# Kernel tuning notes

Hardware: AMD Instinct MI355X
Metric: run time of the kernel (lower is better)

The kernel has to match this reference:

```python
import jax, jax.numpy as jnp
import numpy as np

H = 8          # num_heads
DIM = 1024     # embed dim
DH = DIM // H // 2   # per-branch head dim = 64
B, N = 2, 2048
LAMBDA_INIT = 0.5
COS_MIN, COS_MAX = 0.0, 15.0
ALPHA = 0.5            # cos_head_residual_alpha
COS_EPS = 1e-6
RMS_EPS = 1e-5
# raw init so that sigmoid(raw) = (cos_scale_init - min)/(max - min) = 1/15
RAW_INIT = float(np.log((1.0/15.0) / (1.0 - 1.0/15.0)))


def setup_inputs() -> dict:
    key = jax.random.key(0)
    ks = jax.random.split(key, 10)
    s = 1.0 / np.sqrt(DIM)
    return {
        "x": jax.random.normal(ks[0], (B, N, DIM), jnp.float32),
        "Wq": jax.random.normal(ks[1], (DIM, DIM), jnp.float32) * s,
        "Wk": jax.random.normal(ks[2], (DIM, DIM), jnp.float32) * s,
        "Wv": jax.random.normal(ks[3], (DIM, DIM), jnp.float32) * s,
        "Wo": jax.random.normal(ks[4], (DIM, DIM), jnp.float32) * s,
        "bo": jnp.zeros((DIM,), jnp.float32),
        "lambda_q1": jax.random.normal(ks[5], (DH,), jnp.float32) * 0.1,
        "lambda_k1": jax.random.normal(ks[6], (DH,), jnp.float32) * 0.1,
        "lambda_q2": jax.random.normal(ks[7], (DH,), jnp.float32) * 0.1,
        "lambda_k2": jax.random.normal(ks[8], (DH,), jnp.float32) * 0.1,
        "delta_gain": jax.random.normal(ks[9], (H,), jnp.float32) * 0.1,
        "cos_head_delta": jnp.zeros((H,), jnp.float32),
        "cos_logit_scale_raw": jnp.float32(RAW_INIT),
        "subln_weight": jnp.ones((2 * DH,), jnp.float32),
    }


def _l2norm(t):
    # F.normalize: x / max(||x||_2, eps)
    return t / jnp.maximum(jnp.linalg.norm(t, axis=-1, keepdims=True), COS_EPS)


def reference(x, Wq, Wk, Wv, Wo, bo,
              lambda_q1, lambda_k1, lambda_q2, lambda_k2,
              delta_gain, cos_head_delta, cos_logit_scale_raw, subln_weight):
    b, n, c = x.shape
    # projections (torch Linear: x @ W.T)
    q = (x @ Wq.T).reshape(b, n, H, 2, DH).transpose(0, 2, 3, 1, 4)  # (B,H,2,N,Dh)
    k = (x @ Wk.T).reshape(b, n, H, 2, DH).transpose(0, 2, 3, 1, 4)
    v = (x @ Wv.T).reshape(b, n, H, 2 * DH).transpose(0, 2, 1, 3)    # (B,H,N,2Dh)
    q1, q2 = q[:, :, 0], q[:, :, 1]
    k1, k2 = k[:, :, 0], k[:, :, 1]

    # smooth-bounded cosine logit scale with per-head residual
    gscale = COS_MIN + (COS_MAX - COS_MIN) * jax.nn.sigmoid(cos_logit_scale_raw)
    head_delta = cos_head_delta - cos_head_delta.mean()
    cos_scale = (gscale * (1.0 + ALPHA * jnp.tanh(head_delta))).reshape(1, H, 1, 1)

    L1 = jnp.einsum('bhnd,bhmd->bhnm', _l2norm(q1), _l2norm(k1)) * cos_scale
    L2 = jnp.einsum('bhnd,bhmd->bhnm', _l2norm(q2), _l2norm(k2)) * cos_scale
    L1 = jnp.nan_to_num(L1)
    L2 = jnp.nan_to_num(L2)

    # tanh-gated interaction between branches
    G = jnp.tanh(delta_gain.reshape(1, H, 1, 1) * (L1 - L2))
    A1 = jax.nn.softmax((L1 + G).astype(jnp.float32), axis=-1).astype(x.dtype)
    A2 = jax.nn.softmax((L2 - G).astype(jnp.float32), axis=-1).astype(x.dtype)

    lambda_1 = jnp.exp(jnp.sum(lambda_q1 * lambda_k1))
    lambda_2 = jnp.exp(jnp.sum(lambda_q2 * lambda_k2))
    lambda_full = (lambda_1 - lambda_2 + LAMBDA_INIT).astype(x.dtype)

    attn = A1 - lambda_full * A2
    y = jnp.einsum('bhnm,bhmd->bhnd', attn, v)  # (B,H,N,2Dh)

    # sub-layer RMSNorm over last dim (2*Dh) with affine weight
    y = y * jax.lax.rsqrt(jnp.mean(y * y, axis=-1, keepdims=True) + RMS_EPS) * subln_weight
    y = y * (1.0 - LAMBDA_INIT)

    y = y.transpose(0, 2, 1, 3).reshape(b, n, c)
    return y @ Wo.T + bo
```

## Files before the change

kernel.cpp:

```cpp
#include <hip/hip_runtime.h>
#include <hip/hip_bf16.h>
#include <cstdint>

typedef __attribute__((ext_vector_type(8))) short short8_t;
typedef __attribute__((ext_vector_type(4))) float f32x4;
typedef __attribute__((ext_vector_type(16))) float f32x16;

#define LOG2E 1.4426950408889634f

__device__ __forceinline__ ushort f2bf(float f){
  union { float f; uint32_t i; } x; x.f = f;
  uint32_t r = x.i + 0x7FFFu + ((x.i >> 16) & 1u);
  return (ushort)(r >> 16);
}
__device__ __forceinline__ float fexp2(float x){
  float r; asm("v_exp_f32 %0, %1" : "=v"(r) : "v"(x)); return r;
}
__device__ __forceinline__ uint32_t cvtpk_bf16(float lo, float hi){
  uint32_t r;
  asm("v_cvt_pk_bf16_f32 %0, %1, %2" : "=v"(r) : "v"(lo), "v"(hi));
  return r;
}
__device__ __forceinline__ void pl32swap(uint32_t &a, uint32_t &b){
  asm volatile("v_permlane32_swap_b32 %0, %1" : "+v"(a), "+v"(b));
}
union PF { uint32_t u[4]; short8_t v; };

__global__ __launch_bounds__(256) void cvt_all_kernel(const float* __restrict__ x,
                                                      const float* __restrict__ Wq,
                                                      const float* __restrict__ Wk,
                                                      const float* __restrict__ Wv,
                                                      const float* __restrict__ Wo,
                                                      ushort* __restrict__ xb,
                                                      ushort* __restrict__ wqb,
                                                      ushort* __restrict__ wkb,
                                                      ushort* __restrict__ wvb,
                                                      ushort* __restrict__ wob){
  int bid = blockIdx.x;
  const float* s; ushort* d; int i;
  if (bid < 4096){ s = x; d = xb; i = bid * 256 + threadIdx.x; }
  else {
    int sel = (bid - 4096) >> 10;
    s = sel == 0 ? Wq : sel == 1 ? Wk : sel == 2 ? Wv : Wo;
    d = sel == 0 ? wqb : sel == 1 ? wkb : sel == 2 ? wvb : wob;
    i = ((bid - 4096) & 1023) * 256 + threadIdx.x;
  }
  float4 v = ((const float4*)s)[i];
  ushort4 o;
  o.x = f2bf(v.x); o.y = f2bf(v.y); o.z = f2bf(v.z); o.w = f2bf(v.w);
  ((ushort4*)d)[i] = o;
}

__global__ void prep_kernel(const float* __restrict__ lq1, const float* __restrict__ lk1,
                            const float* __restrict__ lq2, const float* __restrict__ lk2,
                            const float* __restrict__ dgain, const float* __restrict__ chd,
                            const float* __restrict__ rawp, float* __restrict__ sc){
  int lane = threadIdx.x;
  float p1 = lq1[lane] * lk1[lane];
  float p2 = lq2[lane] * lk2[lane];
  #pragma unroll
  for (int o = 1; o < 64; o <<= 1){
    p1 += __shfl_xor(p1, o, 64);
    p2 += __shfl_xor(p2, o, 64);
  }
  if (lane == 0) sc[24] = expf(p1) - expf(p2) + 0.5f;
  if (lane < 8){
    float m = 0.f;
    for (int i = 0; i < 8; i++) m += chd[i];
    m *= 0.125f;
    float gs = 15.f / (1.f + expf(-rawp[0]));
    float cs = gs * (1.f + 0.5f * tanhf(chd[lane] - m));
    sc[lane]      = LOG2E * cs;
    sc[8 + lane]  = LOG2E * (cs + 1.f);
    sc[16 + lane] = 2.f * dgain[lane];
  }
}

__global__ __launch_bounds__(256) void gemm_qkv(const ushort* __restrict__ A,
                                                const ushort* __restrict__ wqb,
                                                const ushort* __restrict__ wkb,
                                                const ushort* __restrict__ wvb,
                                                ushort* __restrict__ Qs,
                                                ushort* __restrict__ Kn,
                                                ushort* __restrict__ Vt,
                                                const float* __restrict__ sc){
  constexpr int N = 1024, K = 1024;
  __shared__ ushort As[128*32];
  __shared__ ushort Bs[128*32];
  const int z = blockIdx.z;
  const ushort* Bm = z == 0 ? wqb : (z == 1 ? wkb : wvb);
  const int t = threadIdx.x;
  const int lane = t & 63;
  const int w = t >> 6;
  const int wr = w >> 1, wc = w & 1;
  const long Ar0 = (long)blockIdx.x * 128;
  const long Br0 = (long)blockIdx.y * 128;
  const int r15 = lane & 15;
  const int kb = (lane >> 4) * 8;

  f32x4 acc[4][4];
  #pragma unroll
  for (int m = 0; m < 4; m++)
    #pragma unroll
    for (int n = 0; n < 4; n++) acc[m][n] = (f32x4){0.f, 0.f, 0.f, 0.f};

  for (int k0 = 0; k0 < K; k0 += 32){
    __syncthreads();
    #pragma unroll
    for (int r = 0; r < 2; r++){
      int li = r * 256 + t;
      int row = li >> 2;
      int col = (li & 3) * 8;
      __builtin_amdgcn_global_load_lds(
        (const __attribute__((address_space(1))) uint32_t*)(A + (Ar0 + row) * K + k0 + col),
        (__attribute__((address_space(3))) uint32_t*)(As + li * 8), 16, 0, 0);
      __builtin_amdgcn_global_load_lds(
        (const __attribute__((address_space(1))) uint32_t*)(Bm + (Br0 + row) * K + k0 + col),
        (__attribute__((address_space(3))) uint32_t*)(Bs + li * 8), 16, 0, 0);
    }
    __syncthreads();
    short8_t af[4], bfv[4];
    #pragma unroll
    for (int m = 0; m < 4; m++) af[m]  = *(const short8_t*)(As + (wr*64 + m*16 + r15)*32 + kb);
    #pragma unroll
    for (int n = 0; n < 4; n++) bfv[n] = *(const short8_t*)(Bs + (wc*64 + n*16 + r15)*32 + kb);
    #pragma unroll
    for (int m = 0; m < 4; m++)
      #pragma unroll
      for (int n = 0; n < 4; n++)
        acc[m][n] = __builtin_amdgcn_mfma_f32_16x16x32_bf16(af[m], bfv[n], acc[m][n], 0, 0, 0);
  }

  const int fr = (lane >> 4) * 4;
  if (z == 2){
    #pragma unroll
    for (int m = 0; m < 4; m++){
      #pragma unroll
      for (int n = 0; n < 4; n++){
        long row0 = Ar0 + wr*64 + m*16 + fr;
        long col  = Br0 + wc*64 + n*16 + r15;
        int bidx = (int)(row0 >> 11);
        int tok  = (int)(row0 & 2047);
        int hh   = (int)(col >> 7);
        int dd   = (int)(col & 127);
        ushort4 pk;
        pk.x = f2bf(acc[m][n][0]); pk.y = f2bf(acc[m][n][1]);
        pk.z = f2bf(acc[m][n][2]); pk.w = f2bf(acc[m][n][3]);
        *(ushort4*)(Vt + ((long)((bidx*8 + hh)*128 + dd))*2048 + tok) = pk;
      }
    }
  } else {
    ushort* dst = (z == 0) ? Qs : Kn;
    const float qsc = (z == 0) ? sc[Br0 >> 7] : 1.f;
    #pragma unroll
    for (int m = 0; m < 4; m++){
      float ss[4] = {0.f, 0.f, 0.f, 0.f};
      #pragma unroll
      for (int n = 0; n < 4; n++)
        #pragma unroll
        for (int r = 0; r < 4; r++) ss[r] = fmaf(acc[m][n][r], acc[m][n][r], ss[r]);
      #pragma unroll
      for (int r = 0; r < 4; r++){
        ss[r] += __shfl_xor(ss[r], 1, 16);
        ss[r] += __shfl_xor(ss[r], 2, 16);
        ss[r] += __shfl_xor(ss[r], 4, 16);
        ss[r] += __shfl_xor(ss[r], 8, 16);
        ss[r] = qsc / fmaxf(sqrtf(ss[r]), 1e-6f);
      }
      long row0 = Ar0 + wr*64 + m*16 + fr;
      #pragma unroll
      for (int n = 0; n < 4; n++){
        long col = Br0 + wc*64 + n*16 + r15;
        #pragma unroll
        for (int r = 0; r < 4; r++)
          dst[(row0 + r) * N + col] = f2bf(acc[m][n][r] * ss[r]);
      }
    }
  }
}

__global__ __launch_bounds__(256) void gemm_o(const ushort* __restrict__ A,
                                              const ushort* __restrict__ Bm,
                                              float* __restrict__ Cout,
                                              const float* __restrict__ bias){
  constexpr int N = 1024, K = 1024;
  __shared__ ushort As[128*32];
  __shared__ ushort Bs[128*32];
  const int t = threadIdx.x;
  const int lane = t & 63;
  const int w = t >> 6;
  const int wr = w >> 1, wc = w & 1;
  const long Ar0 = (long)blockIdx.x * 128;
  const long Br0 = (long)blockIdx.y * 128;
  const int r15 = lane & 15;
  const int kb = (lane >> 4) * 8;

  f32x4 acc[4][4];
  #pragma unroll
  for (int m = 0; m < 4; m++)
    #pragma unroll
    for (int n = 0; n < 4; n++) acc[m][n] = (f32x4){0.f, 0.f, 0.f, 0.f};

  for (int k0 = 0; k0 < K; k0 += 32){
    __syncthreads();
    #pragma unroll
    for (int r = 0; r < 2; r++){
      int li = r * 256 + t;
      int row = li >> 2;
      int col = (li & 3) * 8;
      __builtin_amdgcn_global_load_lds(
        (const __attribute__((address_space(1))) uint32_t*)(A + (Ar0 + row) * K + k0 + col),
        (__attribute__((address_space(3))) uint32_t*)(As + li * 8), 16, 0, 0);
      __builtin_amdgcn_global_load_lds(
        (const __attribute__((address_space(1))) uint32_t*)(Bm + (Br0 + row) * K + k0 + col),
        (__attribute__((address_space(3))) uint32_t*)(Bs + li * 8), 16, 0, 0);
    }
    __syncthreads();
    short8_t af[4], bfv[4];
    #pragma unroll
    for (int m = 0; m < 4; m++) af[m]  = *(const short8_t*)(As + (wr*64 + m*16 + r15)*32 + kb);
    #pragma unroll
    for (int n = 0; n < 4; n++) bfv[n] = *(const short8_t*)(Bs + (wc*64 + n*16 + r15)*32 + kb);
    #pragma unroll
    for (int m = 0; m < 4; m++)
      #pragma unroll
      for (int n = 0; n < 4; n++)
        acc[m][n] = __builtin_amdgcn_mfma_f32_16x16x32_bf16(af[m], bfv[n], acc[m][n], 0, 0, 0);
  }

  const int fr = (lane >> 4) * 4;
  #pragma unroll
  for (int m = 0; m < 4; m++){
    #pragma unroll
    for (int n = 0; n < 4; n++){
      long row0 = Ar0 + wr*64 + m*16 + fr;
      long col  = Br0 + wc*64 + n*16 + r15;
      float bsv = bias[col];
      #pragma unroll
      for (int r = 0; r < 4; r++)
        Cout[(row0 + r) * N + col] = acc[m][n][r] + bsv;
    }
  }
}

__device__ __forceinline__ void stage256(const ushort* __restrict__ Kn,
                                         const ushort* __restrict__ Vt,
                                         long kslice, long vslice, int ktAbs,
                                         ushort* buf, int t){
  #pragma unroll
  for (int r = 0; r < 4; r++){
    int s = r * 256 + t;
    int key = s >> 4, ci = s & 15;
    const ushort* srcK = Kn + kslice + (long)(ktAbs + key) * 1024 + ((ci ^ (key & 15)) * 8);
    __builtin_amdgcn_global_load_lds(
      (const __attribute__((address_space(1))) uint32_t*)srcK,
      (__attribute__((address_space(3))) uint32_t*)(buf + s * 8), 16, 0, 0);
    int dim = s >> 3, ci2 = s & 7;
    const ushort* srcV = Vt + vslice + (long)dim * 2048 + ktAbs + ((ci2 ^ (dim & 7)) * 8);
    __builtin_amdgcn_global_load_lds(
      (const __attribute__((address_space(1))) uint32_t*)srcV,
      (__attribute__((address_space(3))) uint32_t*)(buf + 64*128 + s * 8), 16, 0, 0);
  }
}

__global__ __launch_bounds__(256, 2) void attn5_kernel(
    const ushort* __restrict__ Qs, const ushort* __restrict__ Kn,
    const ushort* __restrict__ Vt, ushort* __restrict__ Yb,
    const float* __restrict__ sc, const float* __restrict__ subw){
  __shared__ ushort KV[2][64*128 + 128*64];
  __shared__ float Zb[2][2][64];
  const int t = threadIdx.x;
  const int w = t >> 6;
  const int l = t & 63;
  const int lo5 = l & 31;
  const int hi = l >> 5;
  const int qt = w >> 1;
  const int kp = w & 1;
  const int bh = blockIdx.y;
  const int b = bh >> 3, h = bh & 7;
  const int q0 = blockIdx.x * 64 + qt * 32;
  const float dgh2 = sc[16 + h];
  const float shl  = sc[8 + h];
  const float lam  = sc[24];

  short8_t qf[8];
  {
    const ushort* qp = Qs + (long)(b*2048 + q0 + lo5) * 1024 + h*128 + hi*8;
    #pragma unroll
    for (int c = 0; c < 2; c++)
      #pragma unroll
      for (int kc = 0; kc < 4; kc++)
        qf[c*4 + kc] = *(const short8_t*)(qp + c*64 + kc*16);
  }

  f32x16 y1a[4], y2a[4];
  #pragma unroll
  for (int nt = 0; nt < 4; nt++)
    #pragma unroll
    for (int i = 0; i < 16; i++){ y1a[nt][i] = 0.f; y2a[nt][i] = 0.f; }
  float Z1 = 0.f, Z2 = 0.f;

  const long kslice = (long)b * 2048 * 1024 + h * 128;
  const long vslice = (long)(b*8 + h) * 128 * 2048;

  for (int kt0 = 0; kt0 < 1024; kt0 += 64){
    __syncthreads();
    stage256(Kn, Vt, kslice, vslice, kt0,        KV[0], t);
    stage256(Kn, Vt, kslice, vslice, 1024 + kt0, KV[1], t);
    __syncthreads();
    const ushort* Ks = KV[kp];
    const ushort* Vs = KV[kp] + 64*128;

    #pragma unroll
    for (int step = 0; step < 2; step++){
      const int key = step*32 + lo5;
      const int krow = key * 128;
      const int ksw = key & 15;
      f32x16 s1, s2;
      #pragma unroll
      for (int i = 0; i < 16; i++){ s1[i] = 0.f; s2[i] = 0.f; }
      #pragma unroll
      for (int kc = 0; kc < 4; kc++){
        short8_t kf = *(const short8_t*)(Ks + krow + (((kc*2 + hi) ^ ksw) * 8));
        s1 = __builtin_amdgcn_mfma_f32_32x32x16_bf16(kf, qf[kc], s1, 0, 0, 0);
      }
      #pragma unroll
      for (int kc = 0; kc < 4; kc++){
        short8_t kf = *(const short8_t*)(Ks + krow + (((8 + kc*2 + hi) ^ ksw) * 8));
        s2 = __builtin_amdgcn_mfma_f32_32x32x16_bf16(kf, qf[4 + kc], s2, 0, 0, 0);
      }

      uint32_t pa1[8], pa2[8];
      #pragma unroll
      for (int ks = 0; ks < 2; ks++){
        #pragma unroll
        for (int u = 0; u < 2; u++){
          const int rr = 8*ks + 2*u;
          float e1[4], e2[4];
          #pragma unroll
          for (int g4 = 0; g4 < 4; g4++){
            const int r = rr + (g4 >> 1)*4 + (g4 & 1);
            float a = s1[r], c = s2[r];
            float e  = fexp2(dgh2 * (a - c));
            float rc = __builtin_amdgcn_rcpf(e + 1.f);
            float gl = fmaf(-2.f * LOG2E, rc, LOG2E);
            float p1 = fexp2(a + gl - shl);
            float p2 = fexp2(c - gl - shl);
            Z1 += p1; Z2 += p2;
            e1[g4] = p1; e2[g4] = p2;
          }
          uint32_t a1 = cvtpk_bf16(e1[0], e1[1]), b1 = cvtpk_bf16(e1[2], e1[3]);
          uint32_t a2 = cvtpk_bf16(e2[0], e2[1]), b2 = cvtpk_bf16(e2[2], e2[3]);
          pl32swap(a1, b1);
          pl32swap(a2, b2);
          pa1[ks*4 + u] = a1; pa1[ks*4 + 2 + u] = b1;
          pa2[ks*4 + u] = a2; pa2[ks*4 + 2 + u] = b2;
        }
      }

      #pragma unroll
      for (int ks = 0; ks < 2; ks++){
        PF f1, f2;
        #pragma unroll
        for (int i = 0; i < 4; i++){ f1.u[i] = pa1[ks*4 + i]; f2.u[i] = pa2[ks*4 + i]; }
        const int ck = step*4 + ks*2 + hi;
        #pragma unroll
        for (int nt = 0; nt < 4; nt++){
          const int dim = nt*32 + lo5;
          short8_t vf = *(const short8_t*)(Vs + dim*64 + ((ck ^ (dim & 7)) * 8));
          y1a[nt] = __builtin_amdgcn_mfma_f32_32x32x16_bf16(f1.v, vf, y1a[nt], 0, 0, 0);
          y2a[nt] = __builtin_amdgcn_mfma_f32_32x32x16_bf16(f2.v, vf, y2a[nt], 0, 0, 0);
        }
      }
    }
  }

  Z1 += __shfl_xor(Z1, 32, 64);
  Z2 += __shfl_xor(Z2, 32, 64);

  __syncthreads();
  float* Mb = (float*)(&KV[0][0]);
  if (kp == 1){
    #pragma unroll
    for (int nt = 0; nt < 4; nt++)
      #pragma unroll
      for (int i = 0; i < 16; i++){
        Mb[(((qt*2 + 0)*4 + nt)*16 + i)*64 + l] = y1a[nt][i];
        Mb[(((qt*2 + 1)*4 + nt)*16 + i)*64 + l] = y2a[nt][i];
      }
    Zb[qt][0][l] = Z1; Zb[qt][1][l] = Z2;
  }
  __syncthreads();
  if (kp == 1) return;

  #pragma unroll
  for (int nt = 0; nt < 4; nt++)
    #pragma unroll
    for (int i = 0; i < 16; i++){
      y1a[nt][i] += Mb[(((qt*2 + 0)*4 + nt)*16 + i)*64 + l];
      y2a[nt][i] += Mb[(((qt*2 + 1)*4 + nt)*16 + i)*64 + l];
    }
  Z1 += Zb[qt][0][l];
  Z2 += Zb[qt][1][l];

  #pragma unroll
  for (int r = 0; r < 16; r++){
    const int qr = (r & 3) + 8*(r >> 2) + 4*hi;
    float z1r = __shfl(Z1, (l & 32) | qr, 64);
    float z2r = __shfl(Z2, (l & 32) | qr, 64);
    float inv1 = 1.f / z1r;
    float inv2 = lam / z2r;
    float yv[4]; float ssq = 0.f;
    #pragma unroll
    for (int nt = 0; nt < 4; nt++){
      yv[nt] = y1a[nt][r]*inv1 - y2a[nt][r]*inv2;
      ssq = fmaf(yv[nt], yv[nt], ssq);
    }
    ssq += __shfl_xor(ssq, 1, 64);
    ssq += __shfl_xor(ssq, 2, 64);
    ssq += __shfl_xor(ssq, 4, 64);
    ssq += __shfl_xor(ssq, 8, 64);
    ssq += __shfl_xor(ssq, 16, 64);
    float rms = rsqrtf(ssq * (1.f / 128.f) + 1e-5f);
    const long tok = (long)b*2048 + q0 + qr;
    ushort* op = Yb + tok*1024 + h*128;
    #pragma unroll
    for (int nt = 0; nt < 4; nt++){
      const int dim = nt*32 + lo5;
      op[dim] = f2bf(yv[nt] * rms * subw[dim] * 0.5f);
    }
  }
}

extern "C" void kernel_launch(void* const* d_in, const int* in_sizes, int n_in,
                              void* d_out, int out_size, void* d_ws, size_t ws_size,
                              hipStream_t stream) {
  const float* x   = (const float*)d_in[0];
  const float* Wq  = (const float*)d_in[1];
  const float* Wk  = (const float*)d_in[2];
  const float* Wv  = (const float*)d_in[3];
  const float* Wo  = (const float*)d_in[4];
  const float* bo  = (const float*)d_in[5];
  const float* lq1 = (const float*)d_in[6];
  const float* lk1 = (const float*)d_in[7];
  const float* lq2 = (const float*)d_in[8];
  const float* lk2 = (const float*)d_in[9];
  const float* dg  = (const float*)d_in[10];
  const float* chd = (const float*)d_in[11];
  const float* raw = (const float*)d_in[12];
  const float* subw= (const float*)d_in[13];
  float* out = (float*)d_out;

  char* ws = (char*)d_ws;
  const size_t MB = 1024 * 1024;
  ushort* xb  = (ushort*)(ws);
  ushort* wqb = (ushort*)(ws + 8 * MB);
  ushort* wkb = wqb + 1024 * 1024;
  ushort* wvb = wkb + 1024 * 1024;
  ushort* wob = wvb + 1024 * 1024;
  ushort* Qs  = (ushort*)(ws + 16 * MB);
  ushort* Kn  = Qs + 4 * 1024 * 1024;
  ushort* Vt  = Kn + 4 * 1024 * 1024;
  ushort* Yb  = Vt + 4 * 1024 * 1024;
  float*  sc  = (float*)(Yb + 4 * 1024 * 1024);

  cvt_all_kernel<<<8192, 256, 0, stream>>>(x, Wq, Wk, Wv, Wo, xb, wqb, wkb, wvb, wob);
  prep_kernel<<<1, 64, 0, stream>>>(lq1, lk1, lq2, lk2, dg, chd, raw, sc);

  gemm_qkv<<<dim3(32, 8, 3), 256, 0, stream>>>(xb, wqb, wkb, wvb, Qs, Kn, Vt, sc);

  attn5_kernel<<<dim3(32, 16), 256, 0, stream>>>(Qs, Kn, Vt, Yb, sc, subw);

  gemm_o<<<dim3(32, 8), 256, 0, stream>>>(Yb, wob, out, bo);
}
```

Baseline: 164.1 us.

## Double-buffer K/V tiles in attention to overlap prefetch with compute

The attention kernel now stages 32-key K/V tiles into two alternating LDS buffers. It issues the async global-to-LDS loads for the next tile right after a single barrier, then computes on the current tile, replacing the old load-then-barrier-then-compute pattern that had two barriers per 64-key step. The V swizzle is reworked for the narrower 32-key tile, and load offsets are precomputed once outside the loop. It also drops the per-head constant log-shift subtraction before exp2. That saves one op per element, but it relies on the bounded cosine logits to avoid overflow.

```diff
diff --git a/kernel.cpp b/kernel.cpp
--- a/kernel.cpp
+++ b/kernel.cpp
@@ -243,31 +243,11 @@
   }
 }
 
-__device__ __forceinline__ void stage256(const ushort* __restrict__ Kn,
-                                         const ushort* __restrict__ Vt,
-                                         long kslice, long vslice, int ktAbs,
-                                         ushort* buf, int t){
-  #pragma unroll
-  for (int r = 0; r < 4; r++){
-    int s = r * 256 + t;
-    int key = s >> 4, ci = s & 15;
-    const ushort* srcK = Kn + kslice + (long)(ktAbs + key) * 1024 + ((ci ^ (key & 15)) * 8);
-    __builtin_amdgcn_global_load_lds(
-      (const __attribute__((address_space(1))) uint32_t*)srcK,
-      (__attribute__((address_space(3))) uint32_t*)(buf + s * 8), 16, 0, 0);
-    int dim = s >> 3, ci2 = s & 7;
-    const ushort* srcV = Vt + vslice + (long)dim * 2048 + ktAbs + ((ci2 ^ (dim & 7)) * 8);
-    __builtin_amdgcn_global_load_lds(
-      (const __attribute__((address_space(1))) uint32_t*)srcV,
-      (__attribute__((address_space(3))) uint32_t*)(buf + 64*128 + s * 8), 16, 0, 0);
-  }
-}
-
-__global__ __launch_bounds__(256, 2) void attn5_kernel(
+__global__ __launch_bounds__(256, 2) void attn6_kernel(
     const ushort* __restrict__ Qs, const ushort* __restrict__ Kn,
     const ushort* __restrict__ Vt, ushort* __restrict__ Yb,
     const float* __restrict__ sc, const float* __restrict__ subw){
-  __shared__ ushort KV[2][64*128 + 128*64];
+  __shared__ ushort KV[2][2][8192];
   __shared__ float Zb[2][2][64];
   const int t = threadIdx.x;
   const int w = t >> 6;
@@ -280,8 +260,8 @@
   const int b = bh >> 3, h = bh & 7;
   const int q0 = blockIdx.x * 64 + qt * 32;
   const float dgh2 = sc[16 + h];
-  const float shl  = sc[8 + h];
   const float lam  = sc[24];
+  const int f2 = (lo5 & 3) ^ ((lo5 >> 2) & 3);
 
   short8_t qf[8];
   {
@@ -303,74 +283,103 @@
   const long kslice = (long)b * 2048 * 1024 + h * 128;
   const long vslice = (long)(b*8 + h) * 128 * 2048;
 
-  for (int kt0 = 0; kt0 < 1024; kt0 += 64){
+  int koff[2], kdst[2], voff[2], vdst[2];
+  #pragma unroll
+  for (int r = 0; r < 2; r++){
+    int c = r * 256 + t;
+    int key = c >> 4, ci = c & 15;
+    kdst[r] = c * 8;
+    koff[r] = key * 1024 + ((ci ^ (key & 15)) * 8);
+    int dim = c >> 2, ci2 = c & 3;
+    int fv = (dim & 3) ^ ((dim >> 2) & 3);
+    vdst[r] = 4096 + c * 8;
+    voff[r] = dim * 2048 + ((ci2 ^ fv) * 8);
+  }
+
+  auto stage = [&](int tileKp, int buf, int ktAbs){
+    const ushort* bk = Kn + kslice + (long)ktAbs * 1024;
+    const ushort* bv = Vt + vslice + ktAbs;
+    ushort* dst = &KV[tileKp][buf][0];
+    #pragma unroll
+    for (int r = 0; r < 2; r++){
+      __builtin_amdgcn_global_load_lds(
+        (const __attribute__((address_space(1))) uint32_t*)(bk + koff[r]),
+        (__attribute__((address_space(3))) uint32_t*)(dst + kdst[r]), 16, 0, 0);
+      __builtin_amdgcn_global_load_lds(
+        (const __attribute__((address_space(1))) uint32_t*)(bv + voff[r]),
+        (__attribute__((address_space(3))) uint32_t*)(dst + vdst[r]), 16, 0, 0);
+    }
+  };
+
+  stage(0, 0, 0);
+  stage(1, 0, 1024);
+  int buf = 0;
+  for (int it = 0; it < 32; it++, buf ^= 1){
     __syncthreads();
-    stage256(Kn, Vt, kslice, vslice, kt0,        KV[0], t);
-    stage256(Kn, Vt, kslice, vslice, 1024 + kt0, KV[1], t);
-    __syncthreads();
-    const ushort* Ks = KV[kp];
-    const ushort* Vs = KV[kp] + 64*128;
-
-    #pragma unroll
-    for (int step = 0; step < 2; step++){
-      const int key = step*32 + lo5;
-      const int krow = key * 128;
-      const int ksw = key & 15;
-      f32x16 s1, s2;
-      #pragma unroll
-      for (int i = 0; i < 16; i++){ s1[i] = 0.f; s2[i] = 0.f; }
-      #pragma unroll
-      for (int kc = 0; kc < 4; kc++){
-        short8_t kf = *(const short8_t*)(Ks + krow + (((kc*2 + hi) ^ ksw) * 8));
-        s1 = __builtin_amdgcn_mfma_f32_32x32x16_bf16(kf, qf[kc], s1, 0, 0, 0);
-      }
-      #pragma unroll
-      for (int kc = 0; kc < 4; kc++){
-        short8_t kf = *(const short8_t*)(Ks + krow + (((8 + kc*2 + hi) ^ ksw) * 8));
-        s2 = __builtin_amdgcn_mfma_f32_32x32x16_bf16(kf, qf[4 + kc], s2, 0, 0, 0);
-      }
-
-      uint32_t pa1[8], pa2[8];
-      #pragma unroll
-      for (int ks = 0; ks < 2; ks++){
+    if (it + 1 < 32){
+      stage(0, buf ^ 1, (it + 1) * 32);
+      stage(1, buf ^ 1, 1024 + (it + 1) * 32);
+    }
+    const ushort* Ks = &KV[kp][buf][0];
+    const ushort* Vs = &KV[kp][buf][4096];
+
+    const int key = lo5;
+    const int krow = key * 128;
+    const int ksw = key & 15;
+    f32x16 s1, s2;
+    #pragma unroll
+    for (int i = 0; i < 16; i++){ s1[i] = 0.f; s2[i] = 0.f; }
+    #pragma unroll
+    for (int kc = 0; kc < 4; kc++){
+      short8_t kf = *(const short8_t*)(Ks + krow + (((kc*2 + hi) ^ ksw) * 8));
+      s1 = __builtin_amdgcn_mfma_f32_32x32x16_bf16(kf, qf[kc], s1, 0, 0, 0);
+    }
+    #pragma unroll
+    for (int kc = 0; kc < 4; kc++){
+      short8_t kf = *(const short8_t*)(Ks + krow + (((8 + kc*2 + hi) ^ ksw) * 8));
+      s2 = __builtin_amdgcn_mfma_f32_32x32x16_bf16(kf, qf[4 + kc], s2, 0, 0, 0);
+    }
+
+    uint32_t pa1[8], pa2[8];
+    #pragma unroll
+    for (int ks = 0; ks < 2; ks++){
+      #pragma unroll
+      for (int u = 0; u < 2; u++){
+        const int rr = 8*ks + 2*u;
+        float e1[4], e2[4];
         #pragma unroll
-        for (int u = 0; u < 2; u++){
-          const int rr = 8*ks + 2*u;
-          float e1[4], e2[4];
-          #pragma unroll
-          for (int g4 = 0; g4 < 4; g4++){
-            const int r = rr + (g4 >> 1)*4 + (g4 & 1);
-            float a = s1[r], c = s2[r];
-            float e  = fexp2(dgh2 * (a - c));
-            float rc = __builtin_amdgcn_rcpf(e + 1.f);
-            float gl = fmaf(-2.f * LOG2E, rc, LOG2E);
-            float p1 = fexp2(a + gl - shl);
-            float p2 = fexp2(c - gl - shl);
-            Z1 += p1; Z2 += p2;
-            e1[g4] = p1; e2[g4] = p2;
-          }
-          uint32_t a1 = cvtpk_bf16(e1[0], e1[1]), b1 = cvtpk_bf16(e1[2], e1[3]);
-          uint32_t a2 = cvtpk_bf16(e2[0], e2[1]), b2 = cvtpk_bf16(e2[2], e2[3]);
-          pl32swap(a1, b1);
-          pl32swap(a2, b2);
-          pa1[ks*4 + u] = a1; pa1[ks*4 + 2 + u] = b1;
-          pa2[ks*4 + u] = a2; pa2[ks*4 + 2 + u] = b2;
+        for (int g4 = 0; g4 < 4; g4++){
+          const int r = rr + (g4 >> 1)*4 + (g4 & 1);
+          float a = s1[r], c = s2[r];
+          float e  = fexp2(dgh2 * (a - c));
+          float rc = __builtin_amdgcn_rcpf(e + 1.f);
+          float gl = fmaf(-2.f * LOG2E, rc, LOG2E);
+          float p1 = fexp2(a + gl);
+          float p2 = fexp2(c - gl);
+          Z1 += p1; Z2 += p2;
+          e1[g4] = p1; e2[g4] = p2;
         }
-      }
-
-      #pragma unroll
-      for (int ks = 0; ks < 2; ks++){
-        PF f1, f2;
-        #pragma unroll
-        for (int i = 0; i < 4; i++){ f1.u[i] = pa1[ks*4 + i]; f2.u[i] = pa2[ks*4 + i]; }
-        const int ck = step*4 + ks*2 + hi;
-        #pragma unroll
-        for (int nt = 0; nt < 4; nt++){
-          const int dim = nt*32 + lo5;
-          short8_t vf = *(const short8_t*)(Vs + dim*64 + ((ck ^ (dim & 7)) * 8));
-          y1a[nt] = __builtin_amdgcn_mfma_f32_32x32x16_bf16(f1.v, vf, y1a[nt], 0, 0, 0);
-          y2a[nt] = __builtin_amdgcn_mfma_f32_32x32x16_bf16(f2.v, vf, y2a[nt], 0, 0, 0);
-        }
+        uint32_t a1 = cvtpk_bf16(e1[0], e1[1]), b1 = cvtpk_bf16(e1[2], e1[3]);
+        uint32_t a2 = cvtpk_bf16(e2[0], e2[1]), b2 = cvtpk_bf16(e2[2], e2[3]);
+        pl32swap(a1, b1);
+        pl32swap(a2, b2);
+        pa1[ks*4 + u] = a1; pa1[ks*4 + 2 + u] = b1;
+        pa2[ks*4 + u] = a2; pa2[ks*4 + 2 + u] = b2;
+      }
+    }
+
+    #pragma unroll
+    for (int ks = 0; ks < 2; ks++){
+      PF pf1, pf2;
+      #pragma unroll
+      for (int i = 0; i < 4; i++){ pf1.u[i] = pa1[ks*4 + i]; pf2.u[i] = pa2[ks*4 + i]; }
+      const int ck = ks*2 + hi;
+      #pragma unroll
+      for (int nt = 0; nt < 4; nt++){
+        const int dim = nt*32 + lo5;
+        short8_t vf = *(const short8_t*)(Vs + dim*32 + ((ck ^ f2) * 8));
+        y1a[nt] = __builtin_amdgcn_mfma_f32_32x32x16_bf16(pf1.v, vf, y1a[nt], 0, 0, 0);
+        y2a[nt] = __builtin_amdgcn_mfma_f32_32x32x16_bf16(pf2.v, vf, y2a[nt], 0, 0, 0);
       }
     }
   }
@@ -379,7 +388,7 @@
   Z2 += __shfl_xor(Z2, 32, 64);
 
   __syncthreads();
-  float* Mb = (float*)(&KV[0][0]);
+  float* Mb = (float*)(&KV[0][0][0]);
   if (kp == 1){
     #pragma unroll
     for (int nt = 0; nt < 4; nt++)
@@ -469,7 +478,7 @@
 
   gemm_qkv<<<dim3(32, 8, 3), 256, 0, stream>>>(xb, wqb, wkb, wvb, Qs, Kn, Vt, sc);
 
-  attn5_kernel<<<dim3(32, 16), 256, 0, stream>>>(Qs, Kn, Vt, Yb, sc, subw);
+  attn6_kernel<<<dim3(32, 16), 256, 0, stream>>>(Qs, Kn, Vt, Yb, sc, subw);
 
   gemm_o<<<dim3(32, 8), 256, 0, stream>>>(Yb, wob, out, bo);
 }
```

Result: no change. 163.4 us (-0.5%).
